# Optimization experiments

Measured on AMD Instinct MI355X. Metric: run time of the kernel, lower is better.

The kernel has to match this reference:

```python
import jax, jax.numpy as jnp
import numpy as np

S = 1024          # tokens (prefill)
DIM = 2560
HEAD_DIM = 128
N_HEADS = 20
N_KV = 5
HPG = N_HEADS // N_KV      # heads per kv group = 4
GS = 128                   # weight-scale group size
THETA = 500000.0
EPS = 1e-05
QKV_OUT = (N_HEADS + 2 * N_KV) * HEAD_DIM  # 3840


def setup_inputs() -> dict:
    key = jax.random.key(0)
    ks = jax.random.split(key, 7)
    x = jax.random.normal(ks[0], (S, DIM), jnp.float32)
    # unpacked int2 (ternary) weights, stored as float for the reference math
    w_qkv = jax.random.randint(ks[1], (QKV_OUT, DIM), -1, 2).astype(jnp.float32)
    ws_qkv = jax.random.uniform(ks[2], (QKV_OUT, DIM // GS), jnp.float32, 0.01, 0.05)
    w_o = jax.random.randint(ks[3], (DIM, N_HEADS * HEAD_DIM), -1, 2).astype(jnp.float32)
    ws_o = jax.random.uniform(ks[4], (DIM, N_HEADS * HEAD_DIM // GS), jnp.float32, 0.01, 0.05)
    q_norm_w = 1.0 + 0.02 * jax.random.normal(ks[5], (HEAD_DIM,), jnp.float32)
    k_norm_w = 1.0 + 0.02 * jax.random.normal(ks[6], (HEAD_DIM,), jnp.float32)
    return {"x": x, "w_qkv": w_qkv, "ws_qkv": ws_qkv, "w_o": w_o, "ws_o": ws_o,
            "q_norm_w": q_norm_w, "k_norm_w": k_norm_w}


def _quant_act(x):
    # per-token symmetric int8 quant: s = 127 / max|x| (clamped)
    s = 127.0 / jnp.clip(jnp.max(jnp.abs(x), axis=-1, keepdims=True), 1e-05, None)
    q = jnp.clip(jnp.round(x * s), -128.0, 127.0)
    return q, s


def _bitlinear(x, w, ws):
    # int8 activation x int2 weight GEMM with per-(out,group) dequant scales
    q, s = _quant_act(x)
    w_dq = w * jnp.repeat(ws, GS, axis=1)        # [out, in]
    return (q @ w_dq.T) / s


def _rmsnorm(x, w):
    return x * jax.lax.rsqrt(jnp.mean(x * x, axis=-1, keepdims=True) + EPS) * w


def _rope(x, cos, sin):
    # x: [S, ..., d]; cos/sin: [S, d//2], interleaved-pair (llama) convention
    d2 = x.shape[-1] // 2
    shape = (x.shape[0],) + (1,) * (x.ndim - 2) + (d2,)
    c = cos.reshape(shape)
    s = sin.reshape(shape)
    xr = x.reshape(x.shape[:-1] + (d2, 2))
    x0, x1 = xr[..., 0], xr[..., 1]
    out = jnp.stack([x0 * c - x1 * s, x0 * s + x1 * c], axis=-1)
    return out.reshape(x.shape)


def reference(x, w_qkv, ws_qkv, w_o, ws_o, q_norm_w, k_norm_w):
    qkv = _bitlinear(x, w_qkv, ws_qkv)                       # [S, 3840]
    q_size = N_HEADS * HEAD_DIM
    k_size = N_KV * HEAD_DIM
    xq = qkv[:, :q_size].reshape(S, N_KV, HPG, HEAD_DIM)     # [S, g, h, d]
    xk = qkv[:, q_size:q_size + k_size].reshape(S, N_KV, HEAD_DIM)
    xv = qkv[:, q_size + k_size:].reshape(S, N_KV, HEAD_DIM)
    xq = _rmsnorm(xq, q_norm_w)
    xk = _rmsnorm(xk, k_norm_w)
    # RoPE (prefill: positions 0..S-1)
    pos = jnp.arange(S, dtype=jnp.float32)
    inv_freq = THETA ** (-jnp.arange(0, HEAD_DIM, 2, dtype=jnp.float32) / HEAD_DIM)
    ang = pos[:, None] * inv_freq[None, :]                   # [S, d/2]
    cos, sin = jnp.cos(ang), jnp.sin(ang)
    xq = _rope(xq, cos, sin)
    xk = _rope(xk, cos, sin)
    # GQA causal flash-attention math
    scale = HEAD_DIM ** -0.5
    scores = jnp.einsum('sghd,tgd->ghst', xq, xk) * scale    # [g, h, S, S]
    causal = jnp.tril(jnp.ones((S, S), bool))
    scores = jnp.where(causal, scores, -1e30)
    attn = jax.nn.softmax(scores, axis=-1)
    out = jnp.einsum('ghst,tgd->sghd', attn, xv).reshape(S, N_HEADS * HEAD_DIM)
    return _bitlinear(out, w_o, ws_o)                        # [S, DIM]
```

## Files before the change

kernel.cpp:

```cpp
#include <hip/hip_runtime.h>
#include <hip/hip_bf16.h>
#include <cstdint>
#include <math.h>

#define SEQ 1024
#define DIM 2560
#define HD 128
#define NH 20
#define NKV 5
#define QKV_OUT 3840
#define GS 128

typedef __bf16 bf16;
typedef __bf16 bf16x4 __attribute__((ext_vector_type(4)));
typedef __bf16 bf16x8 __attribute__((ext_vector_type(8)));
typedef float f32x4 __attribute__((ext_vector_type(4)));

__global__ __launch_bounds__(256) void fused_pre(
    const float* __restrict__ x, bf16* __restrict__ act, float* __restrict__ rs,
    const float* __restrict__ w1, const float* __restrict__ ws1, bf16* __restrict__ o1,
    const float* __restrict__ w2, const float* __restrict__ ws2, bf16* __restrict__ o2,
    long n1_4, long total4) {
  const int tid = threadIdx.x;
  if (blockIdx.x < SEQ) {
    const int row = blockIdx.x;
    const float* xr = x + (size_t)row * DIM;
    float m = 0.f;
    for (int i = tid; i < DIM; i += 256) m = fmaxf(m, fabsf(xr[i]));
    for (int off = 32; off; off >>= 1) m = fmaxf(m, __shfl_xor(m, off));
    __shared__ float red[4];
    __shared__ float s_bc;
    if ((tid & 63) == 0) red[tid >> 6] = m;
    __syncthreads();
    if (tid == 0) {
      float mm = fmaxf(fmaxf(red[0], red[1]), fmaxf(red[2], red[3]));
      mm = fmaxf(mm, 1e-5f);
      s_bc = 127.f / mm;
      rs[row] = mm / 127.f;
    }
    __syncthreads();
    const float s = s_bc;
    bf16* ar = act + (size_t)row * DIM;
    for (int i = tid; i < DIM; i += 256) {
      float q = rintf(xr[i] * s);
      q = fminf(fmaxf(q, -128.f), 127.f);
      ar[i] = (bf16)q;
    }
  } else {
    long i = (long)(blockIdx.x - SEQ) * 256 + tid;
    if (i >= total4) return;
    const float* w; const float* ws; bf16* o; long e;
    if (i < n1_4) { w = w1; ws = ws1; o = o1; e = i * 4; }
    else          { w = w2; ws = ws2; o = o2; e = (i - n1_4) * 4; }
    int row = (int)(e / DIM);
    int k = (int)(e % DIM);
    float sc = ws[(size_t)row * (DIM / GS) + (k / GS)];
    float4 wv = *(const float4*)(w + e);
    bf16x4 ov;
    ov[0] = (bf16)(wv.x * sc);
    ov[1] = (bf16)(wv.y * sc);
    ov[2] = (bf16)(wv.z * sc);
    ov[3] = (bf16)(wv.w * sc);
    *(bf16x4*)(o + e) = ov;
  }
}

__device__ __forceinline__ void gload_lds16(const bf16* g, bf16* l) {
  __builtin_amdgcn_global_load_lds(
      (const __attribute__((address_space(1))) void*)g,
      (__attribute__((address_space(3))) void*)l, 16, 0, 0);
}

template <int BM, int BN>
__global__ __launch_bounds__(256) void gemm_pipe(
    const bf16* __restrict__ A, const bf16* __restrict__ B,
    const float* __restrict__ rs, float* __restrict__ C,
    int N, int K, int Kh, size_t part_stride, int ND, int NN) {
  constexpr int MI = BM / 32;
  constexpr int NW = BN / 32;
  constexpr int APASS = BM / 32;
  constexpr int BPASS = BN / 32;
  __shared__ bf16 As[2][BM * 64];
  __shared__ bf16 Bs[2][BN * 64];
  const int b = (int)blockIdx.x;
  const int mtile = b / ND;
  const int nz = b % ND;
  const int ntile = nz % NN;
  const int z = nz / NN;
  const int tid = threadIdx.x;
  const int w = tid >> 6, l = tid & 63;
  const int row0 = mtile * BM;
  const int col0 = ntile * BN;
  const int wm = (w >> 1) * (BM / 2), wn = (w & 1) * (BN / 2);
  const int lcol = l & 15, quad = l >> 4;
  const int sr = l >> 3, sg = l & 7;
  const bf16* Ag = A + (size_t)row0 * K + (size_t)z * Kh;
  const bf16* Bg = B + (size_t)col0 * K + (size_t)z * Kh;

  f32x4 acc[MI][NW] = {};

#define STAGE_AB(buf, k0)                                                      \
  {                                                                            \
    _Pragma("unroll") for (int i = 0; i < APASS; ++i) {                        \
      int rb = w * (BM / 4) + i * 8;                                           \
      int r = rb + sr;                                                         \
      gload_lds16(Ag + (size_t)r * K + (k0) + ((sg ^ (r & 7)) * 8),            \
                  &As[buf][rb * 64]);                                          \
    }                                                                          \
    _Pragma("unroll") for (int i = 0; i < BPASS; ++i) {                        \
      int rb = w * (BN / 4) + i * 8;                                           \
      int r = rb + sr;                                                         \
      gload_lds16(Bg + (size_t)r * K + (k0) + ((sg ^ (r & 7)) * 8),            \
                  &Bs[buf][rb * 64]);                                          \
    }                                                                          \
  }

  STAGE_AB(0, 0)
  __syncthreads();

  int buf = 0;
  for (int k0 = 0; k0 < Kh; k0 += 64) {
    if (k0 + 64 < Kh) STAGE_AB(buf ^ 1, k0 + 64)
#pragma unroll
    for (int ks = 0; ks < 2; ++ks) {
      bf16x8 af[MI], bff[NW];
#pragma unroll
      for (int mi = 0; mi < MI; ++mi) {
        int R = wm + mi * 16 + lcol;
        af[mi] = *(const bf16x8*)(&As[buf][R * 64 + (((ks * 4 + quad) ^ (R & 7)) * 8)]);
      }
#pragma unroll
      for (int ni = 0; ni < NW; ++ni) {
        int R = wn + ni * 16 + lcol;
        bff[ni] = *(const bf16x8*)(&Bs[buf][R * 64 + (((ks * 4 + quad) ^ (R & 7)) * 8)]);
      }
#pragma unroll
      for (int mi = 0; mi < MI; ++mi)
#pragma unroll
        for (int ni = 0; ni < NW; ++ni)
          acc[mi][ni] = __builtin_amdgcn_mfma_f32_16x16x32_bf16(
              af[mi], bff[ni], acc[mi][ni], 0, 0, 0);
    }
    __syncthreads();
    buf ^= 1;
  }
#undef STAGE_AB

  float* Cp = C + (size_t)z * part_stride;
#pragma unroll
  for (int mi = 0; mi < MI; ++mi) {
#pragma unroll
    for (int ni = 0; ni < NW; ++ni) {
      int col = col0 + wn + ni * 16 + lcol;
#pragma unroll
      for (int r = 0; r < 4; ++r) {
        int row = row0 + wm + mi * 16 + quad * 4 + r;
        Cp[(size_t)row * N + col] = acc[mi][ni][r] * rs[row];
      }
    }
  }
}

__global__ __launch_bounds__(256) void fused_post(
    const float* __restrict__ qkvA, const float* __restrict__ qkvB,
    const float* __restrict__ qw, const float* __restrict__ kw,
    bf16* __restrict__ Qo, bf16* __restrict__ Ko, bf16* __restrict__ Vt) {
  __shared__ bf16 Ls[64 * 137];
  const int bx = (int)blockIdx.x;
  const int tid = threadIdx.x;
  if (bx < 6400) {
    const int wave = tid >> 6, i = tid & 63;
    const int u = bx * 4 + wave;
    const int t = u & 1023, h = u >> 10;
    const size_t off = (h < NH)
        ? (size_t)t * QKV_OUT + h * HD
        : (size_t)t * QKV_OUT + 2560 + (h - NH) * HD;
    const float* s1 = qkvA + off;
    const float* s2 = qkvB + off;
    float x0 = s1[2 * i] + s2[2 * i];
    float x1 = s1[2 * i + 1] + s2[2 * i + 1];
    float ss = x0 * x0 + x1 * x1;
    for (int off2 = 1; off2 < 64; off2 <<= 1) ss += __shfl_xor(ss, off2);
    float r = rsqrtf(ss * (1.f / 128.f) + 1e-5f);
    const float* wv = (h < NH) ? qw : kw;
    float y0 = x0 * r * wv[2 * i];
    float y1 = x1 * r * wv[2 * i + 1];
    float inv_freq = powf(500000.f, -(float)(2 * i) * (1.f / 128.f));
    float ang = (float)t * inv_freq;
    float sn, cs;
    sincosf(ang, &sn, &cs);
    float o0 = y0 * cs - y1 * sn;
    float o1 = y0 * sn + y1 * cs;
    if (h < NH) {
      bf16* dst = Qo + ((size_t)t * NH + h) * HD + 2 * i;
      dst[0] = (bf16)o0; dst[1] = (bf16)o1;
    } else {
      bf16* dst = Ko + ((size_t)(h - NH) * SEQ + t) * HD + 2 * i;
      dst[0] = (bf16)o0; dst[1] = (bf16)o1;
    }
  } else {
    const int b2 = bx - 6400;
    const int t0 = (b2 & 15) * 64, g = b2 >> 4;
    {
      const int tl = tid >> 4;
      const int d0 = (tid & 15) * 8;
#pragma unroll
      for (int pass = 0; pass < 4; ++pass) {
        int t = pass * 16 + tl;
        size_t off = (size_t)(t0 + t) * QKV_OUT + 3200 + g * HD + d0;
        float4 a = *(const float4*)(qkvA + off);
        float4 b = *(const float4*)(qkvA + off + 4);
        float4 a2 = *(const float4*)(qkvB + off);
        float4 b2v = *(const float4*)(qkvB + off + 4);
        bf16* dst = Ls + t * 137 + d0;
        dst[0] = (bf16)(a.x + a2.x); dst[1] = (bf16)(a.y + a2.y);
        dst[2] = (bf16)(a.z + a2.z); dst[3] = (bf16)(a.w + a2.w);
        dst[4] = (bf16)(b.x + b2v.x); dst[5] = (bf16)(b.y + b2v.y);
        dst[6] = (bf16)(b.z + b2v.z); dst[7] = (bf16)(b.w + b2v.w);
      }
    }
    __syncthreads();
    {
      const int dl = tid >> 3;
      const int tl0 = (tid & 7) * 8;
#pragma unroll
      for (int pass = 0; pass < 4; ++pass) {
        int d = pass * 32 + dl;
        bf16x8 v;
#pragma unroll
        for (int j = 0; j < 8; ++j) v[j] = Ls[(tl0 + j) * 137 + d];
        *(bf16x8*)(Vt + ((size_t)g * HD + d) * SEQ + t0 + tl0) = v;
      }
    }
  }
}

__global__ __launch_bounds__(256, 1) void attn_mfma(
    const bf16* __restrict__ Qb, const bf16* __restrict__ Kb,
    const bf16* __restrict__ Vt, float* __restrict__ Op,
    float* __restrict__ ml) {
  const int p = (int)blockIdx.x;
  int qb, c;
  if (p < 24)      { qb = 31 - p / 3;            c = p % 3; }
  else if (p < 48) { int r = p - 24; qb = 23 - (r >> 1); c = r & 1; }
  else             { qb = 59 - p;                c = 0; }
  const int hp = blockIdx.y;
  const int tid = threadIdx.x;
  const int wave = tid >> 6, lane = tid & 63;
  const int H = (hp >> 1) * 4 + (hp & 1) * 2 + (wave >> 1);
  const int g = H >> 2;
  const int qcol = lane & 15, quad = lane >> 4;
  const int q_tok = qb * 32 + (wave & 1) * 16 + qcol;
  const float scale = 0.08838834764831843f;

  __shared__ bf16 Ks[2][64 * 128];
  __shared__ bf16 Vs[2][128 * 64];

  const bf16* kbase = Kb + (size_t)g * SEQ * HD;
  const bf16* vbase = Vt + (size_t)g * HD * SEQ;

  bf16x8 qf[4];
  {
    const bf16* qp = Qb + ((size_t)q_tok * NH + H) * HD + quad * 8;
#pragma unroll
    for (int kc = 0; kc < 4; ++kc) qf[kc] = *(const bf16x8*)(qp + kc * 32);
  }

  float m_i = -1e30f, l_i = 0.f;
  f32x4 o_acc[8] = {};
  const int kt0 = c * 6;
  int kt_max = kt0 + 5;
  {
    int ktg = (qb * 32 + 31) >> 6;
    if (ktg < kt_max) kt_max = ktg;
  }

  const int k_r = lane >> 4, k_g = lane & 15;
  const int v_r = lane >> 3, v_g = lane & 7;

#define STAGE(buf, key0)                                                       \
  {                                                                            \
    _Pragma("unroll") for (int p2 = 0; p2 < 4; ++p2) {                         \
      int r0 = wave * 16 + p2 * 4;                                             \
      int r = r0 + k_r;                                                        \
      gload_lds16(kbase + (size_t)((key0) + r) * HD + ((k_g ^ (r & 15)) * 8),  \
                  &Ks[buf][r0 * 128]);                                         \
    }                                                                          \
    _Pragma("unroll") for (int p2 = 0; p2 < 4; ++p2) {                         \
      int r0 = wave * 32 + p2 * 8;                                             \
      int r = r0 + v_r;                                                        \
      gload_lds16(vbase + (size_t)r * SEQ + (key0) + ((v_g ^ (r & 7)) * 8),    \
                  &Vs[buf][r0 * 64]);                                          \
    }                                                                          \
  }

  STAGE(0, kt0 * 64)

  for (int kt = kt0; kt <= kt_max; ++kt) {
    const int key0 = kt * 64;
    __syncthreads();
    if (kt < kt_max) STAGE((kt + 1) & 1, key0 + 64)
    const bf16* Kt = Ks[kt & 1];
    const bf16* Vtile = Vs[kt & 1];

    bf16x8 kf[4][4];
#pragma unroll
    for (int mg = 0; mg < 4; ++mg) {
      const int R = mg * 16 + qcol;
      const bf16* krow = Kt + R * 128;
#pragma unroll
      for (int kc = 0; kc < 4; ++kc)
        kf[mg][kc] = *(const bf16x8*)(krow + (((kc * 4 + quad) ^ (R & 15)) * 8));
    }
    f32x4 s[4];
#pragma unroll
    for (int mg = 0; mg < 4; ++mg) {
      f32x4 acc = {0.f, 0.f, 0.f, 0.f};
#pragma unroll
      for (int kc = 0; kc < 4; ++kc)
        acc = __builtin_amdgcn_mfma_f32_16x16x32_bf16(kf[mg][kc], qf[kc], acc, 0, 0, 0);
      s[mg] = acc;
    }

    bf16x8 vf[8][2];
#pragma unroll
    for (int mg2 = 0; mg2 < 8; ++mg2) {
      const int R = mg2 * 16 + qcol;
      const bf16* vrow = Vtile + R * 64;
#pragma unroll
      for (int cc = 0; cc < 2; ++cc) {
        int g8a = cc * 8 + quad;
        int g8b = cc * 8 + 4 + quad;
        bf16x4 v0 = *(const bf16x4*)(vrow + ((g8a >> 1) ^ (R & 7)) * 8 + (g8a & 1) * 4);
        bf16x4 v1 = *(const bf16x4*)(vrow + ((g8b >> 1) ^ (R & 7)) * 8 + (g8b & 1) * 4);
#pragma unroll
        for (int j = 0; j < 4; ++j) { vf[mg2][cc][j] = v0[j]; vf[mg2][cc][j + 4] = v1[j]; }
      }
    }

    float mt = -1e30f;
#pragma unroll
    for (int mg = 0; mg < 4; ++mg)
#pragma unroll
      for (int r = 0; r < 4; ++r) {
        int key = key0 + mg * 16 + quad * 4 + r;
        float v = (key <= q_tok) ? s[mg][r] * scale : -1e30f;
        s[mg][r] = v;
        mt = fmaxf(mt, v);
      }
    mt = fmaxf(mt, __shfl_xor(mt, 16));
    mt = fmaxf(mt, __shfl_xor(mt, 32));
    float mnew = fmaxf(m_i, mt);
    float alpha = __expf(m_i - mnew);
    float ps = 0.f;
#pragma unroll
    for (int mg = 0; mg < 4; ++mg)
#pragma unroll
      for (int r = 0; r < 4; ++r) {
        float pv = __expf(s[mg][r] - mnew);
        s[mg][r] = pv;
        ps += pv;
      }
    ps += __shfl_xor(ps, 16);
    ps += __shfl_xor(ps, 32);
    l_i = l_i * alpha + ps;
    m_i = mnew;
#pragma unroll
    for (int mg2 = 0; mg2 < 8; ++mg2)
#pragma unroll
      for (int r = 0; r < 4; ++r) o_acc[mg2][r] *= alpha;

    bf16x8 pb[2];
#pragma unroll
    for (int cc = 0; cc < 2; ++cc)
#pragma unroll
      for (int j = 0; j < 8; ++j)
        pb[cc][j] = (bf16)s[cc * 2 + (j >> 2)][j & 3];

#pragma unroll
    for (int mg2 = 0; mg2 < 8; ++mg2) {
      f32x4 acc = o_acc[mg2];
#pragma unroll
      for (int cc = 0; cc < 2; ++cc)
        acc = __builtin_amdgcn_mfma_f32_16x16x32_bf16(vf[mg2][cc], pb[cc], acc, 0, 0, 0);
      o_acc[mg2] = acc;
    }
  }
#undef STAGE

  float* op = Op + ((size_t)c * SEQ + q_tok) * DIM + (size_t)H * HD + quad * 4;
#pragma unroll
  for (int mg2 = 0; mg2 < 8; ++mg2)
    *(f32x4*)(op + mg2 * 16) = o_acc[mg2];
  if (lane < 16) {
    size_t mloff = (((size_t)c * SEQ + q_tok) * NH + H) * 2;
    ml[mloff] = m_i;
    ml[mloff + 1] = l_i;
  }
}

__global__ __launch_bounds__(256) void merge_quant(
    const float* __restrict__ Op, const float* __restrict__ ml,
    bf16* __restrict__ act, float* __restrict__ rs) {
  const int t = blockIdx.x;
  const int tid = threadIdx.x;
  const int nc = (((t | 31) >> 6) / 6) + 1;
  __shared__ float sw[3][NH];
  __shared__ float red[4];
  __shared__ float s_bc;
  if (tid < NH) {
    const size_t base = ((size_t)t * NH + tid) * 2;
    const size_t cs = (size_t)SEQ * NH * 2;
    float m0 = ml[base], l0 = ml[base + 1];
    float m1 = 0.f, l1 = 0.f, m2 = 0.f, l2 = 0.f;
    float M = m0;
    if (nc > 1) { m1 = ml[base + cs];     l1 = ml[base + cs + 1];     M = fmaxf(M, m1); }
    if (nc > 2) { m2 = ml[base + 2 * cs]; l2 = ml[base + 2 * cs + 1]; M = fmaxf(M, m2); }
    float w0 = __expf(m0 - M), w1 = 0.f, w2 = 0.f;
    float L = w0 * l0;
    if (nc > 1) { w1 = __expf(m1 - M); L += w1 * l1; }
    if (nc > 2) { w2 = __expf(m2 - M); L += w2 * l2; }
    const float invL = 1.f / L;
    sw[0][tid] = w0 * invL;
    sw[1][tid] = w1 * invL;
    sw[2][tid] = w2 * invL;
  }
  __syncthreads();
  float vals[10];
  float amax = 0.f;
  const float* ob = Op + (size_t)t * DIM;
  const size_t cs = (size_t)SEQ * DIM;
#pragma unroll
  for (int j = 0; j < 10; ++j) {
    int d = j * 256 + tid;
    int h = d >> 7;
    float v = ob[d] * sw[0][h];
    if (nc > 1) v += ob[d + cs] * sw[1][h];
    if (nc > 2) v += ob[d + 2 * cs] * sw[2][h];
    vals[j] = v;
    amax = fmaxf(amax, fabsf(v));
  }
  for (int off = 32; off; off >>= 1) amax = fmaxf(amax, __shfl_xor(amax, off));
  if ((tid & 63) == 0) red[tid >> 6] = amax;
  __syncthreads();
  if (tid == 0) {
    float mm = fmaxf(fmaxf(red[0], red[1]), fmaxf(red[2], red[3]));
    mm = fmaxf(mm, 1e-5f);
    s_bc = 127.f / mm;
    rs[t] = mm / 127.f;
  }
  __syncthreads();
  const float s = s_bc;
  bf16* ar = act + (size_t)t * DIM;
#pragma unroll
  for (int j = 0; j < 10; ++j) {
    float q = rintf(vals[j] * s);
    q = fminf(fmaxf(q, -128.f), 127.f);
    ar[j * 256 + tid] = (bf16)q;
  }
}

extern "C" void kernel_launch(void* const* d_in, const int* in_sizes, int n_in,
                              void* d_out, int out_size, void* d_ws, size_t ws_size,
                              hipStream_t stream) {
  const float* x      = (const float*)d_in[0];
  const float* w_qkv  = (const float*)d_in[1];
  const float* ws_qkv = (const float*)d_in[2];
  const float* w_o    = (const float*)d_in[3];
  const float* ws_o   = (const float*)d_in[4];
  const float* qnw    = (const float*)d_in[5];
  const float* knw    = (const float*)d_in[6];
  float* out = (float*)d_out;

  char* p = (char*)d_ws;
  bf16*  act1 = (bf16*)p;  p += (size_t)SEQ * DIM * 2;
  float* rs1  = (float*)p; p += 4096;
  bf16*  wqdq = (bf16*)p;  p += (size_t)QKV_OUT * DIM * 2;
  bf16*  wodq = (bf16*)p;  p += (size_t)DIM * DIM * 2;
  float* qkvA = (float*)p; p += (size_t)SEQ * QKV_OUT * 4;
  float* qkvB = (float*)p; p += (size_t)SEQ * QKV_OUT * 4;
  bf16*  Qb   = (bf16*)p;  p += (size_t)SEQ * NH * HD * 2;
  bf16*  Kb   = (bf16*)p;  p += (size_t)NKV * SEQ * HD * 2;
  bf16*  Vt   = (bf16*)p;  p += (size_t)NKV * HD * SEQ * 2;
  bf16*  act2 = (bf16*)p;  p += (size_t)SEQ * DIM * 2;
  float* rs2  = (float*)p; p += 4096;

  float* Opart = qkvA;
  float* mlbuf = (float*)act1;

  {
    long n1_4 = (long)QKV_OUT * DIM / 4;
    long total4 = n1_4 + (long)DIM * DIM / 4;
    int dq_blocks = (int)((total4 + 255) / 256);
    fused_pre<<<SEQ + dq_blocks, 256, 0, stream>>>(
        x, act1, rs1, w_qkv, ws_qkv, wqdq, w_o, ws_o, wodq, n1_4, total4);
  }
  gemm_pipe<128, 128><<<480, 256, 0, stream>>>(
      act1, wqdq, rs1, qkvA, QKV_OUT, DIM, DIM / 2, (size_t)SEQ * QKV_OUT, 60, 30);
  fused_post<<<6480, 256, 0, stream>>>(qkvA, qkvB, qnw, knw, Qb, Kb, Vt);
  attn_mfma<<<dim3(60, 10), 256, 0, stream>>>(Qb, Kb, Vt, Opart, mlbuf);
  merge_quant<<<SEQ, 256, 0, stream>>>(Opart, mlbuf, act2, rs2);
  gemm_pipe<64, 64><<<640, 256, 0, stream>>>(
      act2, wodq, rs2, out, DIM, DIM, DIM, 0, 40, 40);
}
```

Measured before the change: 226.1 us.

## Split attention KV into four chunks, split-K output GEMM, precompute RoPE table

Attention work is now split into up to four KV chunks per query block (80 blocks instead of 60), and merge_quant combines up to four partials. The output projection GEMM switches to 128x128 tiles with a 4-way split-K, followed by a new reduction kernel. RoPE cos/sin values are computed once per token and frequency in fused_pre, replacing per-head sincos in fused_post, and the qkv loads in fused_post are vectorised. These changes aim for better CU occupancy and less redundant transcendental math. The cost is extra partial-sum buffers, extra memory traffic and one more kernel launch.

```diff
diff --git a/kernel.cpp b/kernel.cpp
--- a/kernel.cpp
+++ b/kernel.cpp
@@ -20,7 +20,7 @@
     const float* __restrict__ x, bf16* __restrict__ act, float* __restrict__ rs,
     const float* __restrict__ w1, const float* __restrict__ ws1, bf16* __restrict__ o1,
     const float* __restrict__ w2, const float* __restrict__ ws2, bf16* __restrict__ o2,
-    long n1_4, long total4) {
+    float* __restrict__ rope, long n1_4, long total4) {
   const int tid = threadIdx.x;
   if (blockIdx.x < SEQ) {
     const int row = blockIdx.x;
@@ -48,20 +48,31 @@
     }
   } else {
     long i = (long)(blockIdx.x - SEQ) * 256 + tid;
-    if (i >= total4) return;
-    const float* w; const float* ws; bf16* o; long e;
-    if (i < n1_4) { w = w1; ws = ws1; o = o1; e = i * 4; }
-    else          { w = w2; ws = ws2; o = o2; e = (i - n1_4) * 4; }
-    int row = (int)(e / DIM);
-    int k = (int)(e % DIM);
-    float sc = ws[(size_t)row * (DIM / GS) + (k / GS)];
-    float4 wv = *(const float4*)(w + e);
-    bf16x4 ov;
-    ov[0] = (bf16)(wv.x * sc);
-    ov[1] = (bf16)(wv.y * sc);
-    ov[2] = (bf16)(wv.z * sc);
-    ov[3] = (bf16)(wv.w * sc);
-    *(bf16x4*)(o + e) = ov;
+    if (i < total4) {
+      const float* w; const float* ws; bf16* o; long e;
+      if (i < n1_4) { w = w1; ws = ws1; o = o1; e = i * 4; }
+      else          { w = w2; ws = ws2; o = o2; e = (i - n1_4) * 4; }
+      int row = (int)(e / DIM);
+      int k = (int)(e % DIM);
+      float sc = ws[(size_t)row * (DIM / GS) + (k / GS)];
+      float4 wv = *(const float4*)(w + e);
+      bf16x4 ov;
+      ov[0] = (bf16)(wv.x * sc);
+      ov[1] = (bf16)(wv.y * sc);
+      ov[2] = (bf16)(wv.z * sc);
+      ov[3] = (bf16)(wv.w * sc);
+      *(bf16x4*)(o + e) = ov;
+    } else {
+      long u = i - total4;
+      if (u >= (long)SEQ * 64) return;
+      int t = (int)(u >> 6), fi = (int)(u & 63);
+      float inv_freq = powf(500000.f, -(float)(2 * fi) * (1.f / 128.f));
+      float ang = (float)t * inv_freq;
+      float sn, cs;
+      sincosf(ang, &sn, &cs);
+      rope[u * 2] = cs;
+      rope[u * 2 + 1] = sn;
+    }
   }
 }
 
@@ -161,9 +172,24 @@
   }
 }
 
+__global__ __launch_bounds__(256) void reduce_k4(
+    const float* __restrict__ P, float* __restrict__ out) {
+  const size_t i = (size_t)blockIdx.x * 256 + threadIdx.x;
+  const size_t cs4 = (size_t)SEQ * DIM / 4;
+  const f32x4* p = (const f32x4*)P;
+  f32x4 v = p[i];
+  f32x4 a = p[i + cs4];
+  f32x4 b = p[i + 2 * cs4];
+  f32x4 d = p[i + 3 * cs4];
+#pragma unroll
+  for (int j = 0; j < 4; ++j) v[j] = v[j] + a[j] + b[j] + d[j];
+  *((f32x4*)out + i) = v;
+}
+
 __global__ __launch_bounds__(256) void fused_post(
     const float* __restrict__ qkvA, const float* __restrict__ qkvB,
     const float* __restrict__ qw, const float* __restrict__ kw,
+    const float* __restrict__ rope,
     bf16* __restrict__ Qo, bf16* __restrict__ Ko, bf16* __restrict__ Vt) {
   __shared__ bf16 Ls[64 * 137];
   const int bx = (int)blockIdx.x;
@@ -177,18 +203,18 @@
         : (size_t)t * QKV_OUT + 2560 + (h - NH) * HD;
     const float* s1 = qkvA + off;
     const float* s2 = qkvB + off;
-    float x0 = s1[2 * i] + s2[2 * i];
-    float x1 = s1[2 * i + 1] + s2[2 * i + 1];
+    float2 xa = *(const float2*)(s1 + 2 * i);
+    float2 xb = *(const float2*)(s2 + 2 * i);
+    float x0 = xa.x + xb.x;
+    float x1 = xa.y + xb.y;
     float ss = x0 * x0 + x1 * x1;
     for (int off2 = 1; off2 < 64; off2 <<= 1) ss += __shfl_xor(ss, off2);
     float r = rsqrtf(ss * (1.f / 128.f) + 1e-5f);
     const float* wv = (h < NH) ? qw : kw;
     float y0 = x0 * r * wv[2 * i];
     float y1 = x1 * r * wv[2 * i + 1];
-    float inv_freq = powf(500000.f, -(float)(2 * i) * (1.f / 128.f));
-    float ang = (float)t * inv_freq;
-    float sn, cs;
-    sincosf(ang, &sn, &cs);
+    float2 csn = *(const float2*)(rope + ((size_t)t * 64 + i) * 2);
+    float cs = csn.x, sn = csn.y;
     float o0 = y0 * cs - y1 * sn;
     float o1 = y0 * sn + y1 * cs;
     if (h < NH) {
@@ -241,9 +267,10 @@
     float* __restrict__ ml) {
   const int p = (int)blockIdx.x;
   int qb, c;
-  if (p < 24)      { qb = 31 - p / 3;            c = p % 3; }
-  else if (p < 48) { int r = p - 24; qb = 23 - (r >> 1); c = r & 1; }
-  else             { qb = 59 - p;                c = 0; }
+  if (p < 32)      { qb = 31 - (p >> 2);            c = p & 3; }
+  else if (p < 56) { int r = p - 32; qb = 23 - r / 3; c = r % 3; }
+  else if (p < 72) { int r = p - 56; qb = 15 - (r >> 1); c = r & 1; }
+  else             { qb = 79 - p;                   c = 0; }
   const int hp = blockIdx.y;
   const int tid = threadIdx.x;
   const int wave = tid >> 6, lane = tid & 63;
@@ -268,10 +295,10 @@
 
   float m_i = -1e30f, l_i = 0.f;
   f32x4 o_acc[8] = {};
-  const int kt0 = c * 6;
-  int kt_max = kt0 + 5;
+  const int kt0 = c * 4;
+  int kt_max = kt0 + 3;
   {
-    int ktg = (qb * 32 + 31) >> 6;
+    int ktg = qb >> 1;
     if (ktg < kt_max) kt_max = ktg;
   }
 
@@ -404,26 +431,33 @@
     bf16* __restrict__ act, float* __restrict__ rs) {
   const int t = blockIdx.x;
   const int tid = threadIdx.x;
-  const int nc = (((t | 31) >> 6) / 6) + 1;
-  __shared__ float sw[3][NH];
+  const int nc = (t >> 8) + 1;
+  __shared__ float sw[4][NH];
   __shared__ float red[4];
   __shared__ float s_bc;
   if (tid < NH) {
     const size_t base = ((size_t)t * NH + tid) * 2;
     const size_t cs = (size_t)SEQ * NH * 2;
-    float m0 = ml[base], l0 = ml[base + 1];
-    float m1 = 0.f, l1 = 0.f, m2 = 0.f, l2 = 0.f;
-    float M = m0;
-    if (nc > 1) { m1 = ml[base + cs];     l1 = ml[base + cs + 1];     M = fmaxf(M, m1); }
-    if (nc > 2) { m2 = ml[base + 2 * cs]; l2 = ml[base + 2 * cs + 1]; M = fmaxf(M, m2); }
-    float w0 = __expf(m0 - M), w1 = 0.f, w2 = 0.f;
-    float L = w0 * l0;
-    if (nc > 1) { w1 = __expf(m1 - M); L += w1 * l1; }
-    if (nc > 2) { w2 = __expf(m2 - M); L += w2 * l2; }
+    float m[4], l[4];
+    float M = -1e30f;
+#pragma unroll
+    for (int cc = 0; cc < 4; ++cc) {
+      if (cc < nc) {
+        m[cc] = ml[base + cc * cs];
+        l[cc] = ml[base + cc * cs + 1];
+        M = fmaxf(M, m[cc]);
+      }
+    }
+    float w[4];
+    float L = 0.f;
+#pragma unroll
+    for (int cc = 0; cc < 4; ++cc) {
+      if (cc < nc) { w[cc] = __expf(m[cc] - M); L += w[cc] * l[cc]; }
+      else w[cc] = 0.f;
+    }
     const float invL = 1.f / L;
-    sw[0][tid] = w0 * invL;
-    sw[1][tid] = w1 * invL;
-    sw[2][tid] = w2 * invL;
+#pragma unroll
+    for (int cc = 0; cc < 4; ++cc) sw[cc][tid] = w[cc] * invL;
   }
   __syncthreads();
   float vals[10];
@@ -437,6 +471,7 @@
     float v = ob[d] * sw[0][h];
     if (nc > 1) v += ob[d + cs] * sw[1][h];
     if (nc > 2) v += ob[d + 2 * cs] * sw[2][h];
+    if (nc > 3) v += ob[d + 3 * cs] * sw[3][h];
     vals[j] = v;
     amax = fmaxf(amax, fabsf(v));
   }
@@ -484,22 +519,25 @@
   bf16*  Vt   = (bf16*)p;  p += (size_t)NKV * HD * SEQ * 2;
   bf16*  act2 = (bf16*)p;  p += (size_t)SEQ * DIM * 2;
   float* rs2  = (float*)p; p += 4096;
-
-  float* Opart = qkvA;
-  float* mlbuf = (float*)act1;
+  float* rope = (float*)p; p += (size_t)SEQ * 64 * 2 * 4;
+  float* Opart = (float*)p; p += (size_t)4 * SEQ * DIM * 4;
+  float* mlbuf = (float*)p; p += (size_t)4 * SEQ * NH * 2 * 4;
+  float* g2part = (float*)p; p += (size_t)4 * SEQ * DIM * 4;
 
   {
     long n1_4 = (long)QKV_OUT * DIM / 4;
     long total4 = n1_4 + (long)DIM * DIM / 4;
     int dq_blocks = (int)((total4 + 255) / 256);
-    fused_pre<<<SEQ + dq_blocks, 256, 0, stream>>>(
-        x, act1, rs1, w_qkv, ws_qkv, wqdq, w_o, ws_o, wodq, n1_4, total4);
+    int rope_blocks = (SEQ * 64 + 255) / 256;
+    fused_pre<<<SEQ + dq_blocks + rope_blocks, 256, 0, stream>>>(
+        x, act1, rs1, w_qkv, ws_qkv, wqdq, w_o, ws_o, wodq, rope, n1_4, total4);
   }
   gemm_pipe<128, 128><<<480, 256, 0, stream>>>(
       act1, wqdq, rs1, qkvA, QKV_OUT, DIM, DIM / 2, (size_t)SEQ * QKV_OUT, 60, 30);
-  fused_post<<<6480, 256, 0, stream>>>(qkvA, qkvB, qnw, knw, Qb, Kb, Vt);
-  attn_mfma<<<dim3(60, 10), 256, 0, stream>>>(Qb, Kb, Vt, Opart, mlbuf);
+  fused_post<<<6480, 256, 0, stream>>>(qkvA, qkvB, qnw, knw, rope, Qb, Kb, Vt);
+  attn_mfma<<<dim3(80, 10), 256, 0, stream>>>(Qb, Kb, Vt, Opart, mlbuf);
   merge_quant<<<SEQ, 256, 0, stream>>>(Opart, mlbuf, act2, rs2);
-  gemm_pipe<64, 64><<<640, 256, 0, stream>>>(
-      act2, wodq, rs2, out, DIM, DIM, DIM, 0, 40, 40);
-}
+  gemm_pipe<128, 128><<<640, 256, 0, stream>>>(
+      act2, wodq, rs2, g2part, DIM, DIM, DIM / 4, (size_t)SEQ * DIM, 80, 20);
+  reduce_k4<<<SEQ * DIM / 1024, 256, 0, stream>>>(g2part, out);
+}
```

Result: slower. 235.9 us (+4.3%).
